# Kernel optimization log

Hardware: AMD Instinct MI355X
Metric: run time of the kernel (lower is better)

Reference implementation:

```python
import jax, jax.numpy as jnp
import numpy as np

B = 32        # decoding requests
S = 2048      # max kv length per request (pool slots per request)
H = 32        # query heads
HKV = 8       # kv heads (GQA group = 4)
D = 128       # head dim
SCALE = 0.08838834764831845  # 1/sqrt(D)
NEG = -1e30


def setup_inputs() -> dict:
    key = jax.random.key(0)
    ks = jax.random.split(key, 6)
    q = jax.random.normal(ks[0], (B, H * D), jnp.float32)
    k = jax.random.normal(ks[1], (B, HKV * D), jnp.float32)
    v = jax.random.normal(ks[2], (B, HKV * D), jnp.float32)
    key_buffer = jax.random.normal(ks[3], (B * S, HKV, D), jnp.float32)
    value_buffer = jax.random.normal(ks[4], (B * S, HKV, D), jnp.float32)
    # request b owns contiguous pool slots [b*S, (b+1)*S)
    req_to_token = jnp.arange(B * S, dtype=jnp.int32).reshape(B, S)
    # seq_lens includes the new decode token
    seq_lens = jax.random.randint(ks[5], (B,), S // 2, S + 1, dtype=jnp.int32)
    # new token is written at the last occupied slot of each request
    out_cache_loc = jnp.arange(B, dtype=jnp.int32) * S + seq_lens - 1
    return {"q": q, "k": k, "v": v,
            "key_buffer": key_buffer, "value_buffer": value_buffer,
            "req_to_token": req_to_token, "seq_lens": seq_lens,
            "out_cache_loc": out_cache_loc}


def reference(q, k, v, key_buffer, value_buffer, req_to_token, seq_lens, out_cache_loc):
    # store_kv_cache: write new token's K/V into the paged pool
    k3 = k.reshape(B, HKV, D)
    v3 = v.reshape(B, HKV, D)
    kb = key_buffer.at[out_cache_loc].set(k3)
    vb = value_buffer.at[out_cache_loc].set(v3)
    # token attention: gather KV via page table, masked softmax attention
    K = kb[req_to_token]   # [B, S, HKV, D]
    V = vb[req_to_token]   # [B, S, HKV, D]
    qg = (q * SCALE).reshape(B, HKV, H // HKV, D)      # GQA grouping [B, HKV, G, D]
    scores = jnp.einsum('bkgd,bskd->bkgs', qg, K)      # [B, HKV, G, S]
    valid = jnp.arange(S, dtype=jnp.int32)[None, :] < seq_lens[:, None]  # [B, S]
    scores = jnp.where(valid[:, None, None, :], scores, NEG)
    p = jax.nn.softmax(scores, axis=-1)
    o = jnp.einsum('bkgs,bskd->bkgd', p, V)            # [B, HKV, G, D]
    return o.reshape(B, H * D)
```

## Files before the change

### kernel.cpp

```cpp
#include <hip/hip_runtime.h>

#define BB 32
#define SS 2048
#define HH 32
#define HKV 8
#define GG 4
#define DD 128
#define SCALE 0.08838834764831845f
#define NSPLIT 4
#define CHUNK (SS / NSPLIT)
#define NWAVES 4
#define PARTIAL_STRIDE 520

__global__ __launch_bounds__(256) void attn_partial(
    const float* __restrict__ q,
    const float* __restrict__ k,
    const float* __restrict__ v,
    const float* __restrict__ key_buffer,
    const float* __restrict__ value_buffer,
    const int* __restrict__ req_to_token,
    const int* __restrict__ seq_lens,
    const int* __restrict__ out_cache_loc,
    float* __restrict__ partials)
{
    const int bid   = blockIdx.x;
    const int b     = bid / (HKV * NSPLIT);
    const int rem   = bid % (HKV * NSPLIT);
    const int h     = rem / NSPLIT;
    const int split = rem % NSPLIT;
    const int tid   = threadIdx.x;
    const int wave  = tid >> 6;
    const int lane  = tid & 63;

    __shared__ float q_lds[GG * DD];
    __shared__ float o_lds[NWAVES][GG][DD];
    __shared__ float m_lds[NWAVES][GG];
    __shared__ float l_lds[NWAVES][GG];

    const int seq_len = seq_lens[b];
    const int loc     = out_cache_loc[b];

    {
        const float* qb = q + ((size_t)b * HH + h * GG) * DD;
        q_lds[tid]       = qb[tid] * SCALE;
        q_lds[tid + 256] = qb[tid + 256] * SCALE;
    }
    __syncthreads();

    const int start = split * CHUNK;
    const int end_  = min(start + CHUNK, seq_len);
    float* pbase = partials + (size_t)bid * PARTIAL_STRIDE;

    if (start >= end_) {
        if (tid < GG) { pbase[512 + tid] = -1e30f; pbase[516 + tid] = 0.0f; }
        return;
    }

    float m_g[GG], l_g[GG], acc[GG][4];
    #pragma unroll
    for (int g = 0; g < GG; ++g) {
        m_g[g] = -1e30f; l_g[g] = 0.0f;
        acc[g][0] = acc[g][1] = acc[g][2] = acc[g][3] = 0.0f;
    }

    const int hp = lane >> 5;
    const int dq = lane & 31;
    const int* rt = req_to_token + (size_t)b * SS;
    const float4* q4 = (const float4*)q_lds;
    const float4* kfresh = (const float4*)(k + ((size_t)b * HKV + h) * DD);
    const float4* vfresh = (const float4*)(v + ((size_t)b * HKV + h) * DD);

    for (int base = start + wave * 64; base < end_; base += NWAVES * 64) {
        int  p     = base + lane;
        bool valid = p < end_;
        int  pp    = valid ? p : (end_ - 1);
        int  tok   = rt[pp];
        const float4* krow = (pp == seq_len - 1)
            ? kfresh
            : (const float4*)(key_buffer + ((size_t)tok * HKV + h) * DD);

        float sc[GG] = {0.f, 0.f, 0.f, 0.f};
        #pragma unroll 8
        for (int d4 = 0; d4 < DD / 4; ++d4) {
            float4 kv = krow[d4];
            #pragma unroll
            for (int g = 0; g < GG; ++g) {
                float4 qv = q4[g * (DD / 4) + d4];
                sc[g] += kv.x * qv.x + kv.y * qv.y + kv.z * qv.z + kv.w * qv.w;
            }
        }
        if (!valid) { sc[0] = sc[1] = sc[2] = sc[3] = -1e30f; }

        float pv[GG];
        #pragma unroll
        for (int g = 0; g < GG; ++g) {
            float cm = sc[g];
            #pragma unroll
            for (int off = 32; off > 0; off >>= 1)
                cm = fmaxf(cm, __shfl_xor(cm, off));
            float mn    = fmaxf(m_g[g], cm);
            float alpha = __expf(m_g[g] - mn);
            pv[g]       = __expf(sc[g] - mn);
            float cs = pv[g];
            #pragma unroll
            for (int off = 32; off > 0; off >>= 1)
                cs += __shfl_xor(cs, off);
            l_g[g] = l_g[g] * alpha + cs;
            m_g[g] = mn;
            acc[g][0] *= alpha; acc[g][1] *= alpha;
            acc[g][2] *= alpha; acc[g][3] *= alpha;
        }

        int nvalid = min(64, end_ - base);
        int npairs = (nvalid + 1) >> 1;
        #pragma unroll 4
        for (int j = 0; j < npairs; ++j) {
            int   s     = 2 * j + hp;
            int   tok_s = __shfl(tok, s);
            float p0    = __shfl(pv[0], s);
            float p1    = __shfl(pv[1], s);
            float p2    = __shfl(pv[2], s);
            float p3    = __shfl(pv[3], s);
            const float4* vrow = (tok_s == loc)
                ? vfresh
                : (const float4*)(value_buffer + ((size_t)tok_s * HKV + h) * DD);
            float4 vv = vrow[dq];
            acc[0][0] += p0 * vv.x; acc[0][1] += p0 * vv.y;
            acc[0][2] += p0 * vv.z; acc[0][3] += p0 * vv.w;
            acc[1][0] += p1 * vv.x; acc[1][1] += p1 * vv.y;
            acc[1][2] += p1 * vv.z; acc[1][3] += p1 * vv.w;
            acc[2][0] += p2 * vv.x; acc[2][1] += p2 * vv.y;
            acc[2][2] += p2 * vv.z; acc[2][3] += p2 * vv.w;
            acc[3][0] += p3 * vv.x; acc[3][1] += p3 * vv.y;
            acc[3][2] += p3 * vv.z; acc[3][3] += p3 * vv.w;
        }
    }

    #pragma unroll
    for (int g = 0; g < GG; ++g) {
        #pragma unroll
        for (int c = 0; c < 4; ++c)
            acc[g][c] += __shfl_xor(acc[g][c], 32);
    }

    if (lane < 32) {
        #pragma unroll
        for (int g = 0; g < GG; ++g)
            ((float4*)o_lds[wave][g])[dq] =
                make_float4(acc[g][0], acc[g][1], acc[g][2], acc[g][3]);
    }
    if (lane == 0) {
        #pragma unroll
        for (int g = 0; g < GG; ++g) {
            m_lds[wave][g] = m_g[g];
            l_lds[wave][g] = l_g[g];
        }
    }
    __syncthreads();

    {
        int g  = tid >> 6;
        int d0 = (tid & 63) * 2;
        float M = -1e30f;
        #pragma unroll
        for (int w = 0; w < NWAVES; ++w) M = fmaxf(M, m_lds[w][g]);
        float den = 0.f, o0 = 0.f, o1 = 0.f;
        #pragma unroll
        for (int w = 0; w < NWAVES; ++w) {
            float wgt = __expf(m_lds[w][g] - M);
            den += wgt * l_lds[w][g];
            o0  += wgt * o_lds[w][g][d0];
            o1  += wgt * o_lds[w][g][d0 + 1];
        }
        pbase[g * DD + d0]     = o0;
        pbase[g * DD + d0 + 1] = o1;
        if ((tid & 63) == 0) { pbase[512 + g] = M; pbase[516 + g] = den; }
    }
}

__global__ __launch_bounds__(128) void attn_combine(
    const float* __restrict__ partials, float* __restrict__ out)
{
    const int bh = blockIdx.x;
    const int d  = threadIdx.x;
    const int b  = bh / HKV;
    const int h  = bh % HKV;
    const float* pb = partials + (size_t)bh * NSPLIT * PARTIAL_STRIDE;

    #pragma unroll
    for (int g = 0; g < GG; ++g) {
        float M = -1e30f;
        #pragma unroll
        for (int s = 0; s < NSPLIT; ++s) {
            float l = pb[s * PARTIAL_STRIDE + 516 + g];
            float m = pb[s * PARTIAL_STRIDE + 512 + g];
            if (l > 0.f) M = fmaxf(M, m);
        }
        float den = 0.f, num = 0.f;
        #pragma unroll
        for (int s = 0; s < NSPLIT; ++s) {
            float l = pb[s * PARTIAL_STRIDE + 516 + g];
            float m = pb[s * PARTIAL_STRIDE + 512 + g];
            float wgt = (l > 0.f) ? __expf(m - M) : 0.f;
            den += wgt * l;
            num += wgt * pb[s * PARTIAL_STRIDE + g * DD + d];
        }
        out[((size_t)b * HH + (h * GG + g)) * DD + d] = num / den;
    }
}

extern "C" void kernel_launch(void* const* d_in, const int* in_sizes, int n_in,
                              void* d_out, int out_size, void* d_ws, size_t ws_size,
                              hipStream_t stream)
{
    const float* q  = (const float*)d_in[0];
    const float* k  = (const float*)d_in[1];
    const float* v  = (const float*)d_in[2];
    const float* key_buffer   = (const float*)d_in[3];
    const float* value_buffer = (const float*)d_in[4];
    const int* req_to_token  = (const int*)d_in[5];
    const int* seq_lens      = (const int*)d_in[6];
    const int* out_cache_loc = (const int*)d_in[7];
    float* out      = (float*)d_out;
    float* partials = (float*)d_ws;

    attn_partial<<<BB * HKV * NSPLIT, 256, 0, stream>>>(
        q, k, v, key_buffer, value_buffer,
        req_to_token, seq_lens, out_cache_loc, partials);
    attn_combine<<<BB * HKV, 128, 0, stream>>>(partials, out);
}
```

Measured before the change: 519.6 us.

## Process both wave chunks at once: single-pass softmax with LDS-staged probabilities

After: 557.4 us. +7.3%, slower.

```diff
diff --git a/kernel.cpp b/kernel.cpp
--- a/kernel.cpp
+++ b/kernel.cpp
@@ -7,12 +7,14 @@
 #define GG 4
 #define DD 128
 #define SCALE 0.08838834764831845f
+#define NEG -1e30f
 #define NSPLIT 4
 #define CHUNK (SS / NSPLIT)
 #define NWAVES 4
+#define WPOS (CHUNK / NWAVES)
 #define PARTIAL_STRIDE 520
 
-__global__ __launch_bounds__(256) void attn_partial(
+__global__ __launch_bounds__(256, 4) void attn_partial(
     const float* __restrict__ q,
     const float* __restrict__ k,
     const float* __restrict__ v,
@@ -36,6 +38,8 @@
     __shared__ float o_lds[NWAVES][GG][DD];
     __shared__ float m_lds[NWAVES][GG];
     __shared__ float l_lds[NWAVES][GG];
+    __shared__ float pv_lds[NWAVES][WPOS][GG];
+    __shared__ int   tok_lds[NWAVES][WPOS];
 
     const int seq_len = seq_lens[b];
     const int loc     = out_cache_loc[b];
@@ -52,88 +56,93 @@
     float* pbase = partials + (size_t)bid * PARTIAL_STRIDE;
 
     if (start >= end_) {
-        if (tid < GG) { pbase[512 + tid] = -1e30f; pbase[516 + tid] = 0.0f; }
+        if (tid < GG) { pbase[512 + tid] = NEG; pbase[516 + tid] = 0.0f; }
         return;
     }
 
-    float m_g[GG], l_g[GG], acc[GG][4];
+    const int* rt = req_to_token + (size_t)b * SS;
+    const float4* q4  = (const float4*)q_lds;
+    const float4* kbh = (const float4*)key_buffer   + h * (DD / 4);
+    const float4* vbh = (const float4*)value_buffer + h * (DD / 4);
+    const float4* kfresh = (const float4*)(k + ((size_t)b * HKV + h) * DD);
+    const float4* vfresh = (const float4*)(v + ((size_t)b * HKV + h) * DD);
+
+    const int p0   = start + wave * 64 + lane;
+    const int p1   = p0 + NWAVES * 64;
+    const bool val0 = p0 < end_;
+    const bool val1 = p1 < end_;
+    const int pp0  = val0 ? p0 : end_ - 1;
+    const int pp1  = val1 ? p1 : end_ - 1;
+    const int tok0 = rt[pp0];
+    const int tok1 = rt[pp1];
+    const float4* kr0 = (pp0 == seq_len - 1) ? kfresh : (kbh + tok0 * (HKV * DD / 4));
+    const float4* kr1 = (pp1 == seq_len - 1) ? kfresh : (kbh + tok1 * (HKV * DD / 4));
+
+    float sc0[GG] = {0.f, 0.f, 0.f, 0.f};
+    float sc1[GG] = {0.f, 0.f, 0.f, 0.f};
+    #pragma unroll 4
+    for (int d4 = 0; d4 < DD / 4; ++d4) {
+        float4 k0 = kr0[d4];
+        float4 k1 = kr1[d4];
+        #pragma unroll
+        for (int g = 0; g < GG; ++g) {
+            float4 qv = q4[g * (DD / 4) + d4];
+            sc0[g] += k0.x * qv.x + k0.y * qv.y + k0.z * qv.z + k0.w * qv.w;
+            sc1[g] += k1.x * qv.x + k1.y * qv.y + k1.z * qv.z + k1.w * qv.w;
+        }
+    }
+    if (!val0) { sc0[0] = NEG; sc0[1] = NEG; sc0[2] = NEG; sc0[3] = NEG; }
+    if (!val1) { sc1[0] = NEG; sc1[1] = NEG; sc1[2] = NEG; sc1[3] = NEG; }
+
+    float m_g[GG], l_g[GG], e0[GG], e1[GG];
     #pragma unroll
     for (int g = 0; g < GG; ++g) {
-        m_g[g] = -1e30f; l_g[g] = 0.0f;
-        acc[g][0] = acc[g][1] = acc[g][2] = acc[g][3] = 0.0f;
-    }
+        float m = fmaxf(sc0[g], sc1[g]);
+        #pragma unroll
+        for (int off = 32; off > 0; off >>= 1)
+            m = fmaxf(m, __shfl_xor(m, off));
+        e0[g] = __expf(sc0[g] - m);
+        e1[g] = __expf(sc1[g] - m);
+        float s = e0[g] + e1[g];
+        #pragma unroll
+        for (int off = 32; off > 0; off >>= 1)
+            s += __shfl_xor(s, off);
+        m_g[g] = m; l_g[g] = s;
+    }
+    *(float4*)&pv_lds[wave][lane][0]      = make_float4(e0[0], e0[1], e0[2], e0[3]);
+    *(float4*)&pv_lds[wave][lane + 64][0] = make_float4(e1[0], e1[1], e1[2], e1[3]);
+    tok_lds[wave][lane]      = tok0;
+    tok_lds[wave][lane + 64] = tok1;
+    __syncthreads();
 
     const int hp = lane >> 5;
     const int dq = lane & 31;
-    const int* rt = req_to_token + (size_t)b * SS;
-    const float4* q4 = (const float4*)q_lds;
-    const float4* kfresh = (const float4*)(k + ((size_t)b * HKV + h) * DD);
-    const float4* vfresh = (const float4*)(v + ((size_t)b * HKV + h) * DD);
-
-    for (int base = start + wave * 64; base < end_; base += NWAVES * 64) {
-        int  p     = base + lane;
-        bool valid = p < end_;
-        int  pp    = valid ? p : (end_ - 1);
-        int  tok   = rt[pp];
-        const float4* krow = (pp == seq_len - 1)
-            ? kfresh
-            : (const float4*)(key_buffer + ((size_t)tok * HKV + h) * DD);
-
-        float sc[GG] = {0.f, 0.f, 0.f, 0.f};
-        #pragma unroll 8
-        for (int d4 = 0; d4 < DD / 4; ++d4) {
-            float4 kv = krow[d4];
-            #pragma unroll
-            for (int g = 0; g < GG; ++g) {
-                float4 qv = q4[g * (DD / 4) + d4];
-                sc[g] += kv.x * qv.x + kv.y * qv.y + kv.z * qv.z + kv.w * qv.w;
-            }
-        }
-        if (!valid) { sc[0] = sc[1] = sc[2] = sc[3] = -1e30f; }
-
-        float pv[GG];
-        #pragma unroll
-        for (int g = 0; g < GG; ++g) {
-            float cm = sc[g];
-            #pragma unroll
-            for (int off = 32; off > 0; off >>= 1)
-                cm = fmaxf(cm, __shfl_xor(cm, off));
-            float mn    = fmaxf(m_g[g], cm);
-            float alpha = __expf(m_g[g] - mn);
-            pv[g]       = __expf(sc[g] - mn);
-            float cs = pv[g];
-            #pragma unroll
-            for (int off = 32; off > 0; off >>= 1)
-                cs += __shfl_xor(cs, off);
-            l_g[g] = l_g[g] * alpha + cs;
-            m_g[g] = mn;
-            acc[g][0] *= alpha; acc[g][1] *= alpha;
-            acc[g][2] *= alpha; acc[g][3] *= alpha;
-        }
-
-        int nvalid = min(64, end_ - base);
-        int npairs = (nvalid + 1) >> 1;
-        #pragma unroll 4
-        for (int j = 0; j < npairs; ++j) {
-            int   s     = 2 * j + hp;
-            int   tok_s = __shfl(tok, s);
-            float p0    = __shfl(pv[0], s);
-            float p1    = __shfl(pv[1], s);
-            float p2    = __shfl(pv[2], s);
-            float p3    = __shfl(pv[3], s);
-            const float4* vrow = (tok_s == loc)
-                ? vfresh
-                : (const float4*)(value_buffer + ((size_t)tok_s * HKV + h) * DD);
-            float4 vv = vrow[dq];
-            acc[0][0] += p0 * vv.x; acc[0][1] += p0 * vv.y;
-            acc[0][2] += p0 * vv.z; acc[0][3] += p0 * vv.w;
-            acc[1][0] += p1 * vv.x; acc[1][1] += p1 * vv.y;
-            acc[1][2] += p1 * vv.z; acc[1][3] += p1 * vv.w;
-            acc[2][0] += p2 * vv.x; acc[2][1] += p2 * vv.y;
-            acc[2][2] += p2 * vv.z; acc[2][3] += p2 * vv.w;
-            acc[3][0] += p3 * vv.x; acc[3][1] += p3 * vv.y;
-            acc[3][2] += p3 * vv.z; acc[3][3] += p3 * vv.w;
-        }
+    float acc[GG][4];
+    #pragma unroll
+    for (int g = 0; g < GG; ++g)
+        acc[g][0] = acc[g][1] = acc[g][2] = acc[g][3] = 0.f;
+
+    const int base_w = start + wave * 64;
+    const int v0c = min(max(end_ - base_w, 0), 64);
+    const int v1c = min(max(end_ - (base_w + NWAVES * 64), 0), 64);
+    const int imax   = (v1c > 0) ? 64 + v1c : v0c;
+    const int npairs = (imax + 1) >> 1;
+
+    #pragma unroll 4
+    for (int j = 0; j < npairs; ++j) {
+        int    i     = 2 * j + hp;
+        float4 pw    = *(const float4*)&pv_lds[wave][i][0];
+        int    tok_s = tok_lds[wave][i];
+        const float4* vrow = (tok_s == loc) ? vfresh : (vbh + tok_s * (HKV * DD / 4));
+        float4 vv = vrow[dq];
+        acc[0][0] += pw.x * vv.x; acc[0][1] += pw.x * vv.y;
+        acc[0][2] += pw.x * vv.z; acc[0][3] += pw.x * vv.w;
+        acc[1][0] += pw.y * vv.x; acc[1][1] += pw.y * vv.y;
+        acc[1][2] += pw.y * vv.z; acc[1][3] += pw.y * vv.w;
+        acc[2][0] += pw.z * vv.x; acc[2][1] += pw.z * vv.y;
+        acc[2][2] += pw.z * vv.z; acc[2][3] += pw.z * vv.w;
+        acc[3][0] += pw.w * vv.x; acc[3][1] += pw.w * vv.y;
+        acc[3][2] += pw.w * vv.z; acc[3][3] += pw.w * vv.w;
     }
 
     #pragma unroll
@@ -161,7 +170,7 @@
     {
         int g  = tid >> 6;
         int d0 = (tid & 63) * 2;
-        float M = -1e30f;
+        float M = NEG;
         #pragma unroll
         for (int w = 0; w < NWAVES; ++w) M = fmaxf(M, m_lds[w][g]);
         float den = 0.f, o0 = 0.f, o1 = 0.f;
@@ -189,7 +198,7 @@
 
     #pragma unroll
     for (int g = 0; g < GG; ++g) {
-        float M = -1e30f;
+        float M = NEG;
         #pragma unroll
         for (int s = 0; s < NSPLIT; ++s) {
             float l = pb[s * PARTIAL_STRIDE + 516 + g];
```
